# Performance work log

Measured on AMD Instinct MI355X. Metric: run time of the kernel, lower is better.

## Reference

```python
import jax, jax.numpy as jnp
import numpy as np

H = 32  # LSTM hidden size (hardcoded in module)
N = 2 * H  # attention feature dim = 64


def setup_inputs() -> dict:
    key = jax.random.key(0)
    ks = jax.random.split(key, 16)
    B, T = 4096, 512
    inp = {
        "y_t_1_embed": jax.random.normal(ks[0], (B, 1), jnp.float32),
        "h0": jax.random.normal(ks[1], (1, B, H), jnp.float32),
        "c0": jax.random.normal(ks[2], (1, B, H), jnp.float32),
        "encoder_outputs": jax.random.normal(ks[3], (B, T, N), jnp.float32),
        "encoder_feature": jax.random.normal(ks[4], (B * T, N), jnp.float32),
        # LSTM params (PyTorch layout: gates ordered i, f, g, o)
        "W_ih": jax.random.normal(ks[5], (4 * H, 1), jnp.float32) * 0.1,
        "W_hh": jax.random.normal(ks[6], (4 * H, H), jnp.float32) * 0.1,
        "b_ih": jax.random.normal(ks[7], (4 * H,), jnp.float32) * 0.1,
        "b_hh": jax.random.normal(ks[8], (4 * H,), jnp.float32) * 0.1,
        # attention params
        "W_proj": jax.random.normal(ks[9], (N, N), jnp.float32) * 0.1,
        "b_proj": jax.random.normal(ks[10], (N,), jnp.float32) * 0.1,
        "v_w": jax.random.normal(ks[11], (N,), jnp.float32) * 0.1,
        # output MLP params
        "W1": jax.random.normal(ks[12], (N, 2 * N), jnp.float32) * 0.1,
        "b1": jax.random.normal(ks[13], (N,), jnp.float32) * 0.1,
        "W2": jax.random.normal(ks[14], (1, N), jnp.float32) * 0.1,
        "b2": jax.random.normal(ks[15], (1,), jnp.float32) * 0.1,
    }
    return inp


def _decoder_fwd(y, h0, c0, enc_out, enc_feat,
                 W_ih, W_hh, b_ih, b_hh, W_proj, b_proj, v_w, W1, b1, W2, b2):
    B, T, n = enc_out.shape
    h, c = h0[0], c0[0]  # [B, H]
    # single LSTM step (seq_len == 1)
    gates = y @ W_ih.T + h @ W_hh.T + (b_ih + b_hh)  # [B, 4H]
    i, f, g, o = jnp.split(gates, 4, axis=-1)
    c_new = jax.nn.sigmoid(f) * c + jax.nn.sigmoid(i) * jnp.tanh(g)
    h_new = jax.nn.sigmoid(o) * jnp.tanh(c_new)
    s_t_hat = jnp.concatenate([h_new, c_new], axis=1)  # [B, 2H]
    # additive (Bahdanau) attention
    dec_fea = s_t_hat @ W_proj.T + b_proj  # [B, N]
    e = jnp.tanh(enc_feat.reshape(B, T, n) + dec_fea[:, None, :])  # [B, T, N]
    scores = jnp.einsum("btn,n->bt", e, v_w)
    attn = jax.nn.softmax(scores, axis=-1)  # [B, T]
    c_t = jnp.einsum("bt,btn->bn", attn, enc_out)  # [B, N]
    # output MLP
    out_in = jnp.concatenate([s_t_hat, c_t], axis=1)  # [B, 2N]
    output = (out_in @ W1.T + b1) @ W2.T + b2  # [B, 1]
    return output, h_new[None], c_new[None]


def reference(y_t_1_embed, h0, c0, encoder_outputs, encoder_feature,
              W_ih, W_hh, b_ih, b_hh, W_proj, b_proj, v_w, W1, b1, W2, b2):
    return _decoder_fwd(y_t_1_embed, h0, c0, encoder_outputs, encoder_feature,
                        W_ih, W_hh, b_ih, b_hh, W_proj, b_proj, v_w, W1, b1, W2, b2)
```

## Files before the change

### kernel.cpp

```cpp
#include <hip/hip_runtime.h>

#define HH 32
#define NN 64
#define TMAX 512

__device__ __forceinline__ float sigmoidf_(float x) {
    return 1.0f / (1.0f + __expf(-x));
}
__device__ __forceinline__ float ftanh(float x) {
    x = fminf(fmaxf(x, -10.0f), 10.0f);
    float a = __expf(2.0f * x);
    return (a - 1.0f) / (a + 1.0f);
}

__global__ __launch_bounds__(256) void decoder_fused(
    const float* __restrict__ y, const float* __restrict__ h0, const float* __restrict__ c0,
    const float* __restrict__ enc_out, const float* __restrict__ enc_feat,
    const float* __restrict__ W_ih, const float* __restrict__ W_hh,
    const float* __restrict__ b_ih, const float* __restrict__ b_hh,
    const float* __restrict__ W_proj, const float* __restrict__ b_proj,
    const float* __restrict__ v_w,
    const float* __restrict__ W1, const float* __restrict__ b1,
    const float* __restrict__ W2, const float* __restrict__ b2,
    float* __restrict__ out, int B, int T)
{
    const int b   = blockIdx.x;
    const int tid = threadIdx.x;
    const int lane = tid & 63;
    const int wid  = tid >> 6;

    __shared__ float s_h[HH];
    __shared__ float s_c[HH];
    __shared__ float s_gates[4 * HH];
    __shared__ float s_outin[2 * NN];
    __shared__ float s_decfea[NN];
    __shared__ float s_vw[NN];
    __shared__ float s_scores[TMAX];
    __shared__ float s_red[8];
    __shared__ float s_ct[16 * NN];

    if (tid < HH) {
        s_h[tid] = h0[(size_t)b * HH + tid];
        s_c[tid] = c0[(size_t)b * HH + tid];
    }
    if (tid >= 64 && tid < 128) s_vw[tid - 64] = v_w[tid - 64];
    __syncthreads();

    if (tid < 4 * HH) {
        float acc = y[b] * W_ih[tid] + b_ih[tid] + b_hh[tid];
        const float* wr = W_hh + tid * HH;
        #pragma unroll
        for (int k = 0; k < HH; ++k) acc += wr[k] * s_h[k];
        s_gates[tid] = acc;
    }
    __syncthreads();

    if (tid < HH) {
        float ig = sigmoidf_(s_gates[tid]);
        float fg = sigmoidf_(s_gates[HH + tid]);
        float gg = ftanh(s_gates[2 * HH + tid]);
        float og = sigmoidf_(s_gates[3 * HH + tid]);
        float cn = fg * s_c[tid] + ig * gg;
        float hn = og * ftanh(cn);
        s_outin[tid]      = hn;
        s_outin[HH + tid] = cn;
        out[(size_t)B + (size_t)b * HH + tid]                   = hn;
        out[(size_t)B + (size_t)B * HH + (size_t)b * HH + tid]  = cn;
    }
    __syncthreads();

    if (tid < NN) {
        float acc = b_proj[tid];
        const float* wr = W_proj + tid * NN;
        #pragma unroll
        for (int k = 0; k < NN; ++k) acc += wr[k] * s_outin[k];
        s_decfea[tid] = acc;
    }
    __syncthreads();

    const int tg = tid >> 4;
    const int nc = tid & 15;
    const int n0 = nc * 4;
    const float4* ef = (const float4*)(enc_feat + (size_t)b * T * NN);
    const float vw0 = s_vw[n0], vw1 = s_vw[n0 + 1], vw2 = s_vw[n0 + 2], vw3 = s_vw[n0 + 3];
    const float df0 = s_decfea[n0], df1 = s_decfea[n0 + 1], df2 = s_decfea[n0 + 2], df3 = s_decfea[n0 + 3];

    for (int t0 = 0; t0 < T; t0 += 16) {
        int t = t0 + tg;
        float4 v = ef[t * 16 + nc];
        float p = vw0 * ftanh(v.x + df0) + vw1 * ftanh(v.y + df1)
                + vw2 * ftanh(v.z + df2) + vw3 * ftanh(v.w + df3);
        p += __shfl_xor(p, 1);
        p += __shfl_xor(p, 2);
        p += __shfl_xor(p, 4);
        p += __shfl_xor(p, 8);
        if (nc == 0) s_scores[t] = p;
    }
    __syncthreads();

    float m = -3.4e38f;
    for (int t = tid; t < T; t += 256) m = fmaxf(m, s_scores[t]);
    #pragma unroll
    for (int mask = 32; mask >= 1; mask >>= 1) m = fmaxf(m, __shfl_xor(m, mask));
    if (lane == 0) s_red[wid] = m;
    __syncthreads();
    m = fmaxf(fmaxf(s_red[0], s_red[1]), fmaxf(s_red[2], s_red[3]));

    float lsum = 0.0f;
    for (int t = tid; t < T; t += 256) {
        float e = __expf(s_scores[t] - m);
        s_scores[t] = e;
        lsum += e;
    }
    #pragma unroll
    for (int mask = 32; mask >= 1; mask >>= 1) lsum += __shfl_xor(lsum, mask);
    if (lane == 0) s_red[4 + wid] = lsum;
    __syncthreads();
    const float inv = 1.0f / (s_red[4] + s_red[5] + s_red[6] + s_red[7]);
    for (int t = tid; t < T; t += 256) s_scores[t] *= inv;
    __syncthreads();

    const float4* eo = (const float4*)(enc_out + (size_t)b * T * NN);
    float ax = 0.f, ay = 0.f, az = 0.f, aw = 0.f;
    for (int t0 = 0; t0 < T; t0 += 16) {
        int t = t0 + tg;
        float a = s_scores[t];
        float4 v = eo[t * 16 + nc];
        ax += a * v.x; ay += a * v.y; az += a * v.z; aw += a * v.w;
    }
    s_ct[tg * NN + n0]     = ax;
    s_ct[tg * NN + n0 + 1] = ay;
    s_ct[tg * NN + n0 + 2] = az;
    s_ct[tg * NN + n0 + 3] = aw;
    __syncthreads();

    if (tid < NN) {
        float acc = 0.0f;
        #pragma unroll
        for (int g = 0; g < 16; ++g) acc += s_ct[g * NN + tid];
        s_outin[NN + tid] = acc;
    }
    __syncthreads();

    float v2 = 0.0f;
    if (tid < NN) {
        float acc = b1[tid];
        const float* wr = W1 + tid * 2 * NN;
        #pragma unroll
        for (int k = 0; k < 2 * NN; ++k) acc += wr[k] * s_outin[k];
        v2 = acc * W2[tid];
    }
    if (wid == 0) {
        #pragma unroll
        for (int mask = 32; mask >= 1; mask >>= 1) v2 += __shfl_xor(v2, mask);
        if (tid == 0) out[b] = v2 + b2[0];
    }
}

extern "C" void kernel_launch(void* const* d_in, const int* in_sizes, int n_in,
                              void* d_out, int out_size, void* d_ws, size_t ws_size,
                              hipStream_t stream) {
    const float* y        = (const float*)d_in[0];
    const float* h0       = (const float*)d_in[1];
    const float* c0       = (const float*)d_in[2];
    const float* enc_out  = (const float*)d_in[3];
    const float* enc_feat = (const float*)d_in[4];
    const float* W_ih     = (const float*)d_in[5];
    const float* W_hh     = (const float*)d_in[6];
    const float* b_ih     = (const float*)d_in[7];
    const float* b_hh     = (const float*)d_in[8];
    const float* W_proj   = (const float*)d_in[9];
    const float* b_proj   = (const float*)d_in[10];
    const float* v_w      = (const float*)d_in[11];
    const float* W1       = (const float*)d_in[12];
    const float* b1       = (const float*)d_in[13];
    const float* W2       = (const float*)d_in[14];
    const float* b2       = (const float*)d_in[15];
    float* out = (float*)d_out;

    const int B = in_sizes[0];
    const int T = in_sizes[3] / (B * NN);

    decoder_fused<<<B, 256, 0, stream>>>(
        y, h0, c0, enc_out, enc_feat, W_ih, W_hh, b_ih, b_hh,
        W_proj, b_proj, v_w, W1, b1, W2, b2, out, B, T);
}
```

Baseline: 200.0 us.

## Fuse attention scoring, softmax and context into one streaming pass

Computes unnormalized exp scores and accumulates the weighted encoder outputs and partial sums in the same loop that reads the encoder features, normalizing only at the end. This removes the scores buffer, the separate max/sum/normalize passes and several block barriers, and lets both encoder tensors be loaded concurrently. It drops the max subtraction, relying on tanh-bounded scores times small v_w to avoid exp overflow.

```diff
diff --git a/kernel.cpp b/kernel.cpp
--- a/kernel.cpp
+++ b/kernel.cpp
@@ -2,7 +2,6 @@
 
 #define HH 32
 #define NN 64
-#define TMAX 512
 
 __device__ __forceinline__ float sigmoidf_(float x) {
     return 1.0f / (1.0f + __expf(-x));
@@ -26,22 +25,19 @@
 {
     const int b   = blockIdx.x;
     const int tid = threadIdx.x;
-    const int lane = tid & 63;
-    const int wid  = tid >> 6;
 
     __shared__ float s_h[HH];
-    __shared__ float s_c[HH];
     __shared__ float s_gates[4 * HH];
     __shared__ float s_outin[2 * NN];
     __shared__ float s_decfea[NN];
     __shared__ float s_vw[NN];
-    __shared__ float s_scores[TMAX];
-    __shared__ float s_red[8];
     __shared__ float s_ct[16 * NN];
+    __shared__ float s_l[16];
+    __shared__ float s_cstate[HH];
 
     if (tid < HH) {
-        s_h[tid] = h0[(size_t)b * HH + tid];
-        s_c[tid] = c0[(size_t)b * HH + tid];
+        s_h[tid]      = h0[(size_t)b * HH + tid];
+        s_cstate[tid] = c0[(size_t)b * HH + tid];
     }
     if (tid >= 64 && tid < 128) s_vw[tid - 64] = v_w[tid - 64];
     __syncthreads();
@@ -60,12 +56,12 @@
         float fg = sigmoidf_(s_gates[HH + tid]);
         float gg = ftanh(s_gates[2 * HH + tid]);
         float og = sigmoidf_(s_gates[3 * HH + tid]);
-        float cn = fg * s_c[tid] + ig * gg;
+        float cn = fg * s_cstate[tid] + ig * gg;
         float hn = og * ftanh(cn);
         s_outin[tid]      = hn;
         s_outin[HH + tid] = cn;
-        out[(size_t)B + (size_t)b * HH + tid]                   = hn;
-        out[(size_t)B + (size_t)B * HH + (size_t)b * HH + tid]  = cn;
+        out[(size_t)B + (size_t)b * HH + tid]                  = hn;
+        out[(size_t)B + (size_t)B * HH + (size_t)b * HH + tid] = cn;
     }
     __syncthreads();
 
@@ -82,63 +78,38 @@
     const int nc = tid & 15;
     const int n0 = nc * 4;
     const float4* ef = (const float4*)(enc_feat + (size_t)b * T * NN);
+    const float4* eo = (const float4*)(enc_out  + (size_t)b * T * NN);
     const float vw0 = s_vw[n0], vw1 = s_vw[n0 + 1], vw2 = s_vw[n0 + 2], vw3 = s_vw[n0 + 3];
     const float df0 = s_decfea[n0], df1 = s_decfea[n0 + 1], df2 = s_decfea[n0 + 2], df3 = s_decfea[n0 + 3];
 
+    float ax = 0.f, ay = 0.f, az = 0.f, aw = 0.f, lsum = 0.f;
+    #pragma unroll 2
     for (int t0 = 0; t0 < T; t0 += 16) {
-        int t = t0 + tg;
-        float4 v = ef[t * 16 + nc];
-        float p = vw0 * ftanh(v.x + df0) + vw1 * ftanh(v.y + df1)
-                + vw2 * ftanh(v.z + df2) + vw3 * ftanh(v.w + df3);
+        const int idx = (t0 + tg) * 16 + nc;
+        float4 u = ef[idx];
+        float4 v = eo[idx];
+        float p = vw0 * ftanh(u.x + df0) + vw1 * ftanh(u.y + df1)
+                + vw2 * ftanh(u.z + df2) + vw3 * ftanh(u.w + df3);
         p += __shfl_xor(p, 1);
         p += __shfl_xor(p, 2);
         p += __shfl_xor(p, 4);
         p += __shfl_xor(p, 8);
-        if (nc == 0) s_scores[t] = p;
-    }
-    __syncthreads();
-
-    float m = -3.4e38f;
-    for (int t = tid; t < T; t += 256) m = fmaxf(m, s_scores[t]);
-    #pragma unroll
-    for (int mask = 32; mask >= 1; mask >>= 1) m = fmaxf(m, __shfl_xor(m, mask));
-    if (lane == 0) s_red[wid] = m;
-    __syncthreads();
-    m = fmaxf(fmaxf(s_red[0], s_red[1]), fmaxf(s_red[2], s_red[3]));
-
-    float lsum = 0.0f;
-    for (int t = tid; t < T; t += 256) {
-        float e = __expf(s_scores[t] - m);
-        s_scores[t] = e;
+        float e = __expf(p);
+        ax += e * v.x; ay += e * v.y; az += e * v.z; aw += e * v.w;
         lsum += e;
-    }
-    #pragma unroll
-    for (int mask = 32; mask >= 1; mask >>= 1) lsum += __shfl_xor(lsum, mask);
-    if (lane == 0) s_red[4 + wid] = lsum;
-    __syncthreads();
-    const float inv = 1.0f / (s_red[4] + s_red[5] + s_red[6] + s_red[7]);
-    for (int t = tid; t < T; t += 256) s_scores[t] *= inv;
-    __syncthreads();
-
-    const float4* eo = (const float4*)(enc_out + (size_t)b * T * NN);
-    float ax = 0.f, ay = 0.f, az = 0.f, aw = 0.f;
-    for (int t0 = 0; t0 < T; t0 += 16) {
-        int t = t0 + tg;
-        float a = s_scores[t];
-        float4 v = eo[t * 16 + nc];
-        ax += a * v.x; ay += a * v.y; az += a * v.z; aw += a * v.w;
     }
     s_ct[tg * NN + n0]     = ax;
     s_ct[tg * NN + n0 + 1] = ay;
     s_ct[tg * NN + n0 + 2] = az;
     s_ct[tg * NN + n0 + 3] = aw;
+    if (nc == 0) s_l[tg] = lsum;
     __syncthreads();
 
     if (tid < NN) {
-        float acc = 0.0f;
+        float num = 0.0f, L = 0.0f;
         #pragma unroll
-        for (int g = 0; g < 16; ++g) acc += s_ct[g * NN + tid];
-        s_outin[NN + tid] = acc;
+        for (int g = 0; g < 16; ++g) { num += s_ct[g * NN + tid]; L += s_l[g]; }
+        s_outin[NN + tid] = num / L;
     }
     __syncthreads();
 
@@ -150,7 +121,7 @@
         for (int k = 0; k < 2 * NN; ++k) acc += wr[k] * s_outin[k];
         v2 = acc * W2[tid];
     }
-    if (wid == 0) {
+    if (tid < 64) {
         #pragma unroll
         for (int mask = 32; mask >= 1; mask >>= 1) v2 += __shfl_xor(v2, mask);
         if (tid == 0) out[b] = v2 + b2[0];
```

Result: slower. 213.3 us (+6.6%).
